# Optimization experiments

Measured on AMD Instinct MI355X. Metric: run time of the kernel, lower is better.

Reference implementation:

```python
import jax, jax.numpy as jnp
import numpy as np

B, S, D = 8, 1024, 512          # batch, seq_len, embed_dim
H = 8                            # num_heads
KD = D                           # key_dim = embed_dim (per source)
DM = H * KD                      # internal d_model = 4096
FF = 2048                        # dense_dim
EPS = 1e-3                       # keras LayerNormalization default epsilon


def glorot(key, shape):
    fan_in, fan_out = shape[0], shape[1]
    lim = np.sqrt(6.0 / (fan_in + fan_out)).astype(np.float32)
    return jax.random.uniform(key, shape, jnp.float32, -lim, lim)


def setup_inputs() -> dict:
    key = jax.random.key(0)
    ks = jax.random.split(key, 8)
    return {
        "inputs": jax.random.normal(ks[0], (B, S, D), jnp.float32),
        "w_q": glorot(ks[1], (D, DM)), "b_q": jnp.zeros((DM,), jnp.float32),
        "w_k": glorot(ks[2], (D, DM)), "b_k": jnp.zeros((DM,), jnp.float32),
        "w_v": glorot(ks[3], (D, DM)), "b_v": jnp.zeros((DM,), jnp.float32),
        "w_o": glorot(ks[4], (DM, D)), "b_o": jnp.zeros((D,), jnp.float32),
        "w1": glorot(ks[5], (D, FF)), "b1": jnp.zeros((FF,), jnp.float32),
        "w2": glorot(ks[6], (FF, D)), "b2": jnp.zeros((D,), jnp.float32),
        "g1": jnp.ones((D,), jnp.float32), "beta1": jnp.zeros((D,), jnp.float32),
        "g2": jnp.ones((D,), jnp.float32), "beta2": jnp.zeros((D,), jnp.float32),
    }


def _layernorm(x, gamma, beta):
    mu = jnp.mean(x, axis=-1, keepdims=True)
    var = jnp.mean(jnp.square(x - mu), axis=-1, keepdims=True)
    return (x - mu) * jax.lax.rsqrt(var + EPS) * gamma + beta


def reference(inputs, w_q, b_q, w_k, b_k, w_v, b_v, w_o, b_o,
              w1, b1, w2, b2, g1, beta1, g2, beta2):
    # --- custom multi-head self-attention ---
    q = (inputs @ w_q + b_q).reshape(B, S, H, KD)   # [B,S,H,KD]
    k = (inputs @ w_k + b_k).reshape(B, S, H, KD)
    v = (inputs @ w_v + b_v).reshape(B, S, H, KD)
    scale = jnp.sqrt(jnp.float32(KD))
    scores = jnp.einsum("bqhd,bkhd->bhqk", q, k) / scale   # [B,H,S,S]
    attn = jax.nn.softmax(scores, axis=-1)
    ctx = jnp.einsum("bhqk,bkhd->bqhd", attn, v).reshape(B, S, DM)
    attn_out = ctx @ w_o + b_o                               # [B,S,D]
    # --- residual + LN 1 ---
    proj_in = _layernorm(inputs + attn_out, g1, beta1)
    # --- FFN ---
    ffn = jax.nn.relu(proj_in @ w1 + b1) @ w2 + b2
    # --- residual + LN 2 ---
    return _layernorm(proj_in + ffn, g2, beta2)
```

## Files before the change

### kernel.cpp

```cpp
#include <hip/hip_runtime.h>
#include <stdint.h>

typedef __bf16 bf16_t;
typedef bf16_t bf16x8 __attribute__((ext_vector_type(8)));
typedef float floatx4 __attribute__((ext_vector_type(4)));

__device__ __forceinline__ unsigned short f2bf(float f) {
  union { float f; uint32_t u; } v; v.f = f;
  return (unsigned short)((v.u + 0x7fffu + ((v.u >> 16) & 1u)) >> 16);
}

#define GLD16(g, l)                                                            \
  __builtin_amdgcn_global_load_lds(                                            \
      (const __attribute__((address_space(1))) void*)(g),                      \
      (__attribute__((address_space(3))) void*)(l), 16, 0, 0)

__device__ __forceinline__ void xcd_swizzle(int& bx, int& by) {
  const int nx = gridDim.x;
  const int nwg = nx * gridDim.y;
  int id = blockIdx.y * nx + blockIdx.x;
  const int cpx = nwg >> 3;
  id = (id & 7) * cpx + (id >> 3);
  bx = id % nx;
  by = id / nx;
}

template <int BIAS_MODE, bool RELU, bool OUT_BF16>
__global__ __launch_bounds__(512, 2) void gemm256(
    const unsigned short* __restrict__ A, const unsigned short* __restrict__ Bt,
    void* __restrict__ C, const float* __restrict__ bias, int K, int lda,
    int ldb, int ldc, long sA, long sB, long sC) {
  __shared__ __align__(16) unsigned short As[2][256 * 64];
  __shared__ __align__(16) unsigned short Bs[2][256 * 64];
  int bx, by;
  xcd_swizzle(bx, by);
  const int tid = threadIdx.x;
  const int lane = tid & 63;
  const int wave = tid >> 6;
  const int quad = lane >> 4;
  const int l15 = lane & 15;
  const unsigned short* Ab = A + blockIdx.z * sA + (long)by * 256 * lda;
  const unsigned short* Bb = Bt + blockIdx.z * sB + (long)bx * 256 * ldb;
  const int wm = (wave & 1) << 7;
  const int wn = (wave >> 1) << 6;

  floatx4 acc[8][4] = {};

  const int sr = tid >> 3;
  const int sc = tid & 7;
  const int NT = K >> 6;

  auto stage = [&](int t, int buf) {
    const int kt = t << 6;
#pragma unroll
    for (int i = 0; i < 4; ++i) {
      int r = sr + i * 64;
      int gc = sc ^ (r & 7);
      GLD16(Ab + (long)r * lda + kt + gc * 8,
            &As[buf][(i * 64 + (wave << 3)) * 64]);
    }
#pragma unroll
    for (int i = 0; i < 4; ++i) {
      int r = sr + i * 64;
      int gc = sc ^ (r & 7);
      GLD16(Bb + (long)r * ldb + kt + gc * 8,
            &Bs[buf][(i * 64 + (wave << 3)) * 64]);
    }
  };

  stage(0, 0);
  stage(1, 1);
  asm volatile("s_waitcnt vmcnt(8)\n\ts_barrier" ::: "memory");

  int cur = 0;
  for (int t = 0; t < NT; ++t) {
    const unsigned short* Ap = As[cur];
    const unsigned short* Bp = Bs[cur];
    bf16x8 bF[2][2][2];
#pragma unroll
    for (int jh = 0; jh < 2; ++jh)
#pragma unroll
      for (int j2 = 0; j2 < 2; ++j2)
#pragma unroll
        for (int ks = 0; ks < 2; ++ks) {
          int row = wn + jh * 32 + j2 * 16 + l15;
          int sw = (ks * 4 + quad) ^ (row & 7);
          bF[jh][j2][ks] = *(const bf16x8*)(Bp + row * 64 + sw * 8);
        }
#pragma unroll
    for (int ih = 0; ih < 2; ++ih) {
      bf16x8 aF[4][2];
#pragma unroll
      for (int i4 = 0; i4 < 4; ++i4)
#pragma unroll
        for (int ks = 0; ks < 2; ++ks) {
          int row = wm + ih * 64 + i4 * 16 + l15;
          int sw = (ks * 4 + quad) ^ (row & 7);
          aF[i4][ks] = *(const bf16x8*)(Ap + row * 64 + sw * 8);
        }
#pragma unroll
      for (int jh = 0; jh < 2; ++jh) {
        __builtin_amdgcn_s_setprio(1);
#pragma unroll
        for (int j2 = 0; j2 < 2; ++j2)
#pragma unroll
          for (int i4 = 0; i4 < 4; ++i4)
#pragma unroll
            for (int ks = 0; ks < 2; ++ks)
              acc[ih * 4 + i4][jh * 2 + j2] =
                  __builtin_amdgcn_mfma_f32_16x16x32_bf16(
                      aF[i4][ks], bF[jh][j2][ks],
                      acc[ih * 4 + i4][jh * 2 + j2], 0, 0, 0);
        __builtin_amdgcn_s_setprio(0);
      }
    }
    if (t == NT - 1) break;
    asm volatile("s_waitcnt lgkmcnt(0)\n\ts_barrier" ::: "memory");
    if (t + 2 < NT) {
      stage(t + 2, cur);
      asm volatile("s_waitcnt vmcnt(8)\n\ts_barrier" ::: "memory");
    } else {
      asm volatile("s_waitcnt vmcnt(0)\n\ts_barrier" ::: "memory");
    }
    cur ^= 1;
  }

  const int rl = quad << 2;
  const int cl = l15;
#pragma unroll
  for (int i = 0; i < 8; ++i) {
#pragma unroll
    for (int j = 0; j < 4; ++j) {
#pragma unroll
      for (int rg = 0; rg < 4; ++rg) {
        int row = (by << 8) + wm + i * 16 + rl + rg;
        int col = (bx << 8) + wn + j * 16 + cl;
        float v = acc[i][j][rg];
        if (BIAS_MODE == 1) v += bias[col];
        if (BIAS_MODE == 2) v += bias[row];
        if (RELU) v = fmaxf(v, 0.0f);
        long idx = blockIdx.z * sC + (long)row * ldc + col;
        if (OUT_BF16)
          ((unsigned short*)C)[idx] = f2bf(v);
        else
          ((float*)C)[idx] = v;
      }
    }
  }
}

template <int BIAS_MODE, bool RELU, bool OUT_BF16>
__global__ __launch_bounds__(256, 2) void gemm128p(
    const unsigned short* __restrict__ A, const unsigned short* __restrict__ Bt,
    void* __restrict__ C, const float* __restrict__ bias, int K, int lda,
    int ldb, int ldc, long sA, long sB, long sC) {
  __shared__ __align__(16) unsigned short As[2][128 * 64];
  __shared__ __align__(16) unsigned short Bs[2][128 * 64];
  int bx, by;
  xcd_swizzle(bx, by);
  const int tid = threadIdx.x;
  const int lane = tid & 63;
  const int wave = tid >> 6;
  const int quad = lane >> 4;
  const int l15 = lane & 15;
  const unsigned short* Ab = A + blockIdx.z * sA + (long)by * 128 * lda;
  const unsigned short* Bb = Bt + blockIdx.z * sB + (long)bx * 128 * ldb;
  const int wm = (wave & 1) << 6;
  const int wn = (wave >> 1) << 6;

  floatx4 acc[4][4] = {};

  const int sr = tid >> 3;
  const int sc = tid & 7;
  const int NT = K >> 6;

  auto stage = [&](int t, int buf) {
    const int kt = t << 6;
#pragma unroll
    for (int i = 0; i < 4; ++i) {
      int r = sr + i * 32;
      int gc = sc ^ (r & 7);
      GLD16(Ab + (long)r * lda + kt + gc * 8,
            &As[buf][(i * 32 + (wave << 3)) * 64]);
    }
#pragma unroll
    for (int i = 0; i < 4; ++i) {
      int r = sr + i * 32;
      int gc = sc ^ (r & 7);
      GLD16(Bb + (long)r * ldb + kt + gc * 8,
            &Bs[buf][(i * 32 + (wave << 3)) * 64]);
    }
  };

  stage(0, 0);
  stage(1, 1);
  asm volatile("s_waitcnt vmcnt(8)\n\ts_barrier" ::: "memory");

  int cur = 0;
  for (int t = 0; t < NT; ++t) {
    const unsigned short* Ap = As[cur];
    const unsigned short* Bp = Bs[cur];
#pragma unroll
    for (int ks = 0; ks < 2; ++ks) {
      bf16x8 af[4], bfr[4];
#pragma unroll
      for (int i = 0; i < 4; ++i) {
        int row = wm + i * 16 + l15;
        int ch = (ks * 4 + quad) ^ (row & 7);
        af[i] = *(const bf16x8*)(Ap + row * 64 + ch * 8);
      }
#pragma unroll
      for (int j = 0; j < 4; ++j) {
        int row = wn + j * 16 + l15;
        int ch = (ks * 4 + quad) ^ (row & 7);
        bfr[j] = *(const bf16x8*)(Bp + row * 64 + ch * 8);
      }
      __builtin_amdgcn_s_setprio(1);
#pragma unroll
      for (int i = 0; i < 4; ++i)
#pragma unroll
        for (int j = 0; j < 4; ++j)
          acc[i][j] = __builtin_amdgcn_mfma_f32_16x16x32_bf16(af[i], bfr[j],
                                                              acc[i][j], 0, 0, 0);
      __builtin_amdgcn_s_setprio(0);
    }
    if (t == NT - 1) break;
    asm volatile("s_waitcnt lgkmcnt(0)\n\ts_barrier" ::: "memory");
    if (t + 2 < NT) {
      stage(t + 2, cur);
      asm volatile("s_waitcnt vmcnt(8)\n\ts_barrier" ::: "memory");
    } else {
      asm volatile("s_waitcnt vmcnt(0)\n\ts_barrier" ::: "memory");
    }
    cur ^= 1;
  }

  const int rl = quad << 2;
  const int cl = l15;
#pragma unroll
  for (int i = 0; i < 4; ++i) {
#pragma unroll
    for (int j = 0; j < 4; ++j) {
#pragma unroll
      for (int rg = 0; rg < 4; ++rg) {
        int row = (by << 7) + wm + i * 16 + rl + rg;
        int col = (bx << 7) + wn + j * 16 + cl;
        float v = acc[i][j][rg];
        if (BIAS_MODE == 1) v += bias[col];
        if (BIAS_MODE == 2) v += bias[row];
        if (RELU) v = fmaxf(v, 0.0f);
        long idx = blockIdx.z * sC + (long)row * ldc + col;
        if (OUT_BF16)
          ((unsigned short*)C)[idx] = f2bf(v);
        else
          ((float*)C)[idx] = v;
      }
    }
  }
}

__global__ __launch_bounds__(512, 2) void attn(
    const unsigned short* __restrict__ qk, const unsigned short* __restrict__ vt,
    unsigned short* __restrict__ ctx) {
  __shared__ unsigned short ldsK[2][32 * 512];
  __shared__ unsigned short ldsV[2][32 * 512];
  __shared__ unsigned short ldsP[128 * 40];
  __shared__ float ldsL[128];

  const int tid = threadIdx.x;
  const int lane = tid & 63;
  const int wave = tid >> 6;
  const int quad = lane >> 4;
  const int l15 = lane & 15;
  const int b = blockIdx.x >> 3;
  const int h = blockIdx.x & 7;
  const int qblk = blockIdx.y << 7;
  const float cs = 0.044194173824159216f * 1.4426950408889634f;

  bf16x8 qf[16];
  {
    const unsigned short* qp =
        qk + (long)(b * 1024 + qblk + wave * 16 + l15) * 8192 + h * 512 +
        (quad << 3);
#pragma unroll
    for (int ks = 0; ks < 16; ++ks) qf[ks] = *(const bf16x8*)(qp + ks * 32);
  }

  floatx4 o[32];
#pragma unroll
  for (int i = 0; i < 32; ++i) o[i] = floatx4{0.f, 0.f, 0.f, 0.f};
  floatx4 l_i = floatx4{0.f, 0.f, 0.f, 0.f};

  const int st_d = lane >> 2;
  const int st_kc = ((lane & 3) - (lane >> 3)) & 3;

  {
#pragma unroll
    for (int i = 0; i < 4; ++i) {
      int r = i * 8 + wave;
      int gc = (lane & ~7) | ((lane ^ r) & 7);
      GLD16(qk + (long)(b * 1024 + r) * 8192 + 4096 + h * 512 + gc * 8,
            ldsK[0] + r * 512);
    }
#pragma unroll
    for (int i = 0; i < 4; ++i) {
      int j = i * 8 + wave;
      GLD16(vt + (long)(b * 4096 + h * 512 + j * 16 + st_d) * 1024 + st_kc * 8,
            ldsV[0] + j * 512);
    }
  }
  __syncthreads();

  for (int kt = 0; kt < 32; ++kt) {
    const unsigned short* kb = ldsK[kt & 1];
    const unsigned short* vb = ldsV[kt & 1];
    if (kt + 1 < 32) {
#pragma unroll
      for (int i = 0; i < 4; ++i) {
        int r = i * 8 + wave;
        int gc = (lane & ~7) | ((lane ^ r) & 7);
        GLD16(qk + (long)(b * 1024 + (kt + 1) * 32 + r) * 8192 + 4096 +
                  h * 512 + gc * 8,
              ldsK[(kt + 1) & 1] + r * 512);
      }
#pragma unroll
      for (int i = 0; i < 4; ++i) {
        int j = i * 8 + wave;
        GLD16(vt + (long)(b * 4096 + h * 512 + j * 16 + st_d) * 1024 +
                  (kt + 1) * 32 + st_kc * 8,
              ldsV[(kt + 1) & 1] + j * 512);
      }
    }

    floatx4 s0 = floatx4{0.f, 0.f, 0.f, 0.f}, s1 = floatx4{0.f, 0.f, 0.f, 0.f};
#pragma unroll
    for (int ks = 0; ks < 16; ++ks) {
      int ch = ks * 4 + quad;
      int sw = (ch & ~7) | ((ch ^ l15) & 7);
      bf16x8 k0 = *(const bf16x8*)(kb + l15 * 512 + sw * 8);
      bf16x8 k1 = *(const bf16x8*)(kb + (16 + l15) * 512 + sw * 8);
      s0 = __builtin_amdgcn_mfma_f32_16x16x32_bf16(qf[ks], k0, s0, 0, 0, 0);
      s1 = __builtin_amdgcn_mfma_f32_16x16x32_bf16(qf[ks], k1, s1, 0, 0, 0);
    }

    {
      unsigned short* pw = ldsP + wave * 16 * 40;
      const int rb = quad << 2;
#pragma unroll
      for (int r = 0; r < 4; ++r) {
        float e0 = __builtin_amdgcn_exp2f(s0[r] * cs);
        float e1 = __builtin_amdgcn_exp2f(s1[r] * cs);
        l_i[r] += e0 + e1;
        pw[(rb + r) * 40 + l15] = f2bf(e0);
        pw[(rb + r) * 40 + 16 + l15] = f2bf(e1);
      }
    }
    asm volatile("s_waitcnt lgkmcnt(0)\n\ts_barrier" ::: "memory");

#pragma unroll
    for (int half = 0; half < 2; ++half) {
      bf16x8 pf[4];
#pragma unroll
      for (int q4 = 0; q4 < 4; ++q4)
        pf[q4] = *(const bf16x8*)(ldsP + ((half * 4 + q4) * 16 + l15) * 40 +
                                  (quad << 3));
#pragma unroll
      for (int db = 0; db < 4; ++db) {
        int n = wave * 4 + db;
        bf16x8 vf = *(const bf16x8*)(
            vb + n * 512 + (l15 * 4 + ((quad + (l15 >> 1)) & 3)) * 8);
#pragma unroll
        for (int q4 = 0; q4 < 4; ++q4)
          o[(half * 4 + q4) * 4 + db] = __builtin_amdgcn_mfma_f32_16x16x32_bf16(
              pf[q4], vf, o[(half * 4 + q4) * 4 + db], 0, 0, 0);
      }
    }
    __syncthreads();
  }

#pragma unroll
  for (int r = 0; r < 4; ++r) {
    float rs = l_i[r];
    rs += __shfl_xor(rs, 1);
    rs += __shfl_xor(rs, 2);
    rs += __shfl_xor(rs, 4);
    rs += __shfl_xor(rs, 8);
    if (l15 == 0) ldsL[wave * 16 + (quad << 2) + r] = rs;
  }
  __syncthreads();

#pragma unroll
  for (int qb = 0; qb < 8; ++qb) {
    floatx4 lv = *(const floatx4*)(ldsL + qb * 16 + (quad << 2));
    floatx4 inv;
#pragma unroll
    for (int r = 0; r < 4; ++r) inv[r] = 1.0f / lv[r];
#pragma unroll
    for (int db = 0; db < 4; ++db) {
#pragma unroll
      for (int r = 0; r < 4; ++r) {
        long row = (long)(b * 1024 + qblk + qb * 16 + (quad << 2) + r);
        ctx[row * 4096 + h * 512 + wave * 64 + db * 16 + l15] =
            f2bf(o[qb * 4 + db][r] * inv[r]);
      }
    }
  }
}

template <int NPART, bool WB>
__global__ __launch_bounds__(256) void ln_reduce(
    const float* __restrict__ p, long sP, const float* __restrict__ bias,
    const float* __restrict__ resid, const float* __restrict__ gamma,
    const float* __restrict__ beta, float* __restrict__ of,
    unsigned short* __restrict__ ob) {
  const long row = blockIdx.x;
  const int c = threadIdx.x * 2;
  const float2 rv = ((const float2*)(resid + row * 512))[threadIdx.x];
  float x0 = bias[c] + rv.x;
  float x1 = bias[c + 1] + rv.y;
#pragma unroll
  for (int k = 0; k < NPART; ++k) {
    const float2 a = ((const float2*)(p + k * sP + row * 512))[threadIdx.x];
    x0 += a.x;
    x1 += a.y;
  }
  float s = x0 + x1;
  float ss = x0 * x0 + x1 * x1;
#pragma unroll
  for (int d = 1; d < 64; d <<= 1) {
    s += __shfl_xor(s, d);
    ss += __shfl_xor(ss, d);
  }
  __shared__ float ps[4], pq[4];
  const int wave = threadIdx.x >> 6;
  if ((threadIdx.x & 63) == 0) {
    ps[wave] = s;
    pq[wave] = ss;
  }
  __syncthreads();
  s = ps[0] + ps[1] + ps[2] + ps[3];
  ss = pq[0] + pq[1] + pq[2] + pq[3];
  const float mu = s * (1.0f / 512.0f);
  const float rstd = rsqrtf(ss * (1.0f / 512.0f) - mu * mu + 1e-3f);
  const float y0 = (x0 - mu) * rstd * gamma[c] + beta[c];
  const float y1 = (x1 - mu) * rstd * gamma[c + 1] + beta[c + 1];
  ((float2*)(of + row * 512))[threadIdx.x] = make_float2(y0, y1);
  if (WB) {
    ushort2 o2;
    o2.x = f2bf(y0);
    o2.y = f2bf(y1);
    ((ushort2*)(ob + row * 512))[threadIdx.x] = o2;
  }
}

__global__ __launch_bounds__(256) void cast_bf16(const float* __restrict__ in,
                                                 unsigned short* __restrict__ out,
                                                 int n) {
  int i = (blockIdx.x * 256 + threadIdx.x) * 4;
  if (i < n) {
    float4 v = *(const float4*)(in + i);
    ushort4 o;
    o.x = f2bf(v.x);
    o.y = f2bf(v.y);
    o.z = f2bf(v.z);
    o.w = f2bf(v.w);
    *(ushort4*)(out + i) = o;
  }
}

__global__ __launch_bounds__(256) void transpose_cast(const float* __restrict__ in,
                                                      unsigned short* __restrict__ out,
                                                      int R, int C) {
  __shared__ float tile[32][33];
  const int tx = threadIdx.x & 31, ty = threadIdx.x >> 5;
  const int c0 = blockIdx.x * 32, r0 = blockIdx.y * 32;
#pragma unroll
  for (int i = 0; i < 4; ++i)
    tile[ty + i * 8][tx] = in[(long)(r0 + ty + i * 8) * C + c0 + tx];
  __syncthreads();
#pragma unroll
  for (int i = 0; i < 4; ++i)
    out[(long)(c0 + ty + i * 8) * R + r0 + tx] = f2bf(tile[tx][ty + i * 8]);
}

extern "C" void kernel_launch(void* const* d_in, const int* in_sizes, int n_in,
                              void* d_out, int out_size, void* d_ws,
                              size_t ws_size, hipStream_t stream) {
  const float* x = (const float*)d_in[0];
  const float* w_q = (const float*)d_in[1];
  const float* b_q = (const float*)d_in[2];
  const float* w_k = (const float*)d_in[3];
  const float* b_k = (const float*)d_in[4];
  const float* w_v = (const float*)d_in[5];
  const float* b_v = (const float*)d_in[6];
  const float* w_o = (const float*)d_in[7];
  const float* b_o = (const float*)d_in[8];
  const float* w1 = (const float*)d_in[9];
  const float* b1 = (const float*)d_in[10];
  const float* w2 = (const float*)d_in[11];
  const float* b2 = (const float*)d_in[12];
  const float* g1 = (const float*)d_in[13];
  const float* be1 = (const float*)d_in[14];
  const float* g2 = (const float*)d_in[15];
  const float* be2 = (const float*)d_in[16];
  float* out = (float*)d_out;

  char* ws = (char*)d_ws;
  size_t off = 0;
  auto alloc = [&](size_t n) {
    char* p = ws + off;
    off += (n + 255) & ~(size_t)255;
    return p;
  };
  unsigned short* xb = (unsigned short*)alloc(8192ll * 512 * 2);
  unsigned short* wqk_t = (unsigned short*)alloc(8192ll * 512 * 2);
  unsigned short* wv_t = (unsigned short*)alloc(4096ll * 512 * 2);
  unsigned short* wo_t = (unsigned short*)alloc(512ll * 4096 * 2);
  unsigned short* w1_t = (unsigned short*)alloc(2048ll * 512 * 2);
  unsigned short* w2_t = (unsigned short*)alloc(512ll * 2048 * 2);
  float* bqk = (float*)alloc(8192ll * 4);
  unsigned short* qkb = (unsigned short*)alloc(4096ll * 8192 * 2);
  unsigned short* vtb = (unsigned short*)alloc(4ll * 4096 * 1024 * 2);
  unsigned short* ctxf = (unsigned short*)alloc(8192ll * 4096 * 2);
  float* proj = (float*)alloc(8192ll * 512 * 4);
  unsigned short* projb = xb;
  unsigned short* h1 = qkb;
  float* pOP = (float*)qkb;
  float* pF2 = (float*)ctxf;

  hipMemcpyAsync(bqk, b_q, 4096 * 4, hipMemcpyDeviceToDevice, stream);
  hipMemcpyAsync(bqk + 4096, b_k, 4096 * 4, hipMemcpyDeviceToDevice, stream);

  cast_bf16<<<4096, 256, 0, stream>>>(x, xb, 8192 * 512);
  transpose_cast<<<dim3(128, 16), 256, 0, stream>>>(w_q, wqk_t, 512, 4096);
  transpose_cast<<<dim3(128, 16), 256, 0, stream>>>(w_k, wqk_t + 4096ll * 512, 512, 4096);
  transpose_cast<<<dim3(128, 16), 256, 0, stream>>>(w_v, wv_t, 512, 4096);
  transpose_cast<<<dim3(16, 128), 256, 0, stream>>>(w_o, wo_t, 4096, 512);
  transpose_cast<<<dim3(64, 16), 256, 0, stream>>>(w1, w1_t, 512, 2048);
  transpose_cast<<<dim3(16, 64), 256, 0, stream>>>(w2, w2_t, 2048, 512);

  for (int g = 0; g < 2; ++g) {
    const unsigned short* xg = xb + (long)g * 4096 * 512;
    gemm256<1, false, true><<<dim3(32, 16, 1), 512, 0, stream>>>(
        xg, wqk_t, qkb, bqk, 512, 512, 512, 8192, 0, 0, 0);
    gemm256<2, false, true><<<dim3(4, 16, 4), 512, 0, stream>>>(
        wv_t, xg, vtb, b_v, 512, 512, 512, 1024, 0, 1024ll * 512,
        4096ll * 1024);
    attn<<<dim3(32, 8), 512, 0, stream>>>(qkb, vtb, ctxf + (long)g * 4096 * 4096);
  }
  gemm128p<0, false, false><<<dim3(4, 64, 2), 256, 0, stream>>>(
      ctxf, wo_t, pOP, nullptr, 2048, 4096, 4096, 512, 2048, 2048,
      8192ll * 512);
  ln_reduce<2, true><<<8192, 256, 0, stream>>>(pOP, 8192ll * 512, b_o, x, g1,
                                               be1, proj, projb);
  gemm256<1, true, true><<<dim3(8, 32, 1), 512, 0, stream>>>(
      projb, w1_t, h1, b1, 512, 512, 512, 2048, 0, 0, 0);
  gemm128p<0, false, false><<<dim3(4, 64, 2), 256, 0, stream>>>(
      h1, w2_t, pF2, nullptr, 1024, 2048, 2048, 512, 1024, 1024,
      8192ll * 512);
  ln_reduce<2, false><<<8192, 256, 0, stream>>>(pF2, 8192ll * 512, b2, proj,
                                                g2, be2, out, nullptr);
}
```

Baseline: 479.1 us.

## Store split-K partials in bf16 and hoist V projection out of batch loop

The split-K partial outputs of the output-projection and second FFN GEMMs are now written as bf16 instead of fp32, and the LayerNorm reduce kernel reads and widens them. This halves partial-sum traffic. The V projection is now computed once for all 8 batches in a single larger launch before the loop, with the V buffer doubled in size, which cuts launches and raises the grid size. The cost is bf16 rounding of the partials before they are summed, which adds error ahead of the LayerNorm.

```diff
diff --git a/kernel.cpp b/kernel.cpp
--- a/kernel.cpp
+++ b/kernel.cpp
@@ -8,6 +8,12 @@
 __device__ __forceinline__ unsigned short f2bf(float f) {
   union { float f; uint32_t u; } v; v.f = f;
   return (unsigned short)((v.u + 0x7fffu + ((v.u >> 16) & 1u)) >> 16);
+}
+
+__device__ __forceinline__ float bf2f(unsigned short b) {
+  union { uint32_t u; float f; } v;
+  v.u = (uint32_t)b << 16;
+  return v.f;
 }
 
 #define GLD16(g, l)                                                            \
@@ -409,10 +415,10 @@
 
 template <int NPART, bool WB>
 __global__ __launch_bounds__(256) void ln_reduce(
-    const float* __restrict__ p, long sP, const float* __restrict__ bias,
-    const float* __restrict__ resid, const float* __restrict__ gamma,
-    const float* __restrict__ beta, float* __restrict__ of,
-    unsigned short* __restrict__ ob) {
+    const unsigned short* __restrict__ p, long sP,
+    const float* __restrict__ bias, const float* __restrict__ resid,
+    const float* __restrict__ gamma, const float* __restrict__ beta,
+    float* __restrict__ of, unsigned short* __restrict__ ob) {
   const long row = blockIdx.x;
   const int c = threadIdx.x * 2;
   const float2 rv = ((const float2*)(resid + row * 512))[threadIdx.x];
@@ -420,9 +426,9 @@
   float x1 = bias[c + 1] + rv.y;
 #pragma unroll
   for (int k = 0; k < NPART; ++k) {
-    const float2 a = ((const float2*)(p + k * sP + row * 512))[threadIdx.x];
-    x0 += a.x;
-    x1 += a.y;
+    const ushort2 a = ((const ushort2*)(p + k * sP + row * 512))[threadIdx.x];
+    x0 += bf2f(a.x);
+    x1 += bf2f(a.y);
   }
   float s = x0 + x1;
   float ss = x0 * x0 + x1 * x1;
@@ -520,13 +526,13 @@
   unsigned short* w2_t = (unsigned short*)alloc(512ll * 2048 * 2);
   float* bqk = (float*)alloc(8192ll * 4);
   unsigned short* qkb = (unsigned short*)alloc(4096ll * 8192 * 2);
-  unsigned short* vtb = (unsigned short*)alloc(4ll * 4096 * 1024 * 2);
+  unsigned short* vtb = (unsigned short*)alloc(8ll * 4096 * 1024 * 2);
   unsigned short* ctxf = (unsigned short*)alloc(8192ll * 4096 * 2);
   float* proj = (float*)alloc(8192ll * 512 * 4);
   unsigned short* projb = xb;
   unsigned short* h1 = qkb;
-  float* pOP = (float*)qkb;
-  float* pF2 = (float*)ctxf;
+  unsigned short* pOP = qkb;
+  unsigned short* pF2 = (unsigned short*)ctxf;
 
   hipMemcpyAsync(bqk, b_q, 4096 * 4, hipMemcpyDeviceToDevice, stream);
   hipMemcpyAsync(bqk + 4096, b_k, 4096 * 4, hipMemcpyDeviceToDevice, stream);
@@ -539,23 +545,25 @@
   transpose_cast<<<dim3(64, 16), 256, 0, stream>>>(w1, w1_t, 512, 2048);
   transpose_cast<<<dim3(16, 64), 256, 0, stream>>>(w2, w2_t, 2048, 512);
 
+  gemm256<2, false, true><<<dim3(4, 16, 8), 512, 0, stream>>>(
+      wv_t, xb, vtb, b_v, 512, 512, 512, 1024, 0, 1024ll * 512,
+      4096ll * 1024);
+
   for (int g = 0; g < 2; ++g) {
     const unsigned short* xg = xb + (long)g * 4096 * 512;
     gemm256<1, false, true><<<dim3(32, 16, 1), 512, 0, stream>>>(
         xg, wqk_t, qkb, bqk, 512, 512, 512, 8192, 0, 0, 0);
-    gemm256<2, false, true><<<dim3(4, 16, 4), 512, 0, stream>>>(
-        wv_t, xg, vtb, b_v, 512, 512, 512, 1024, 0, 1024ll * 512,
-        4096ll * 1024);
-    attn<<<dim3(32, 8), 512, 0, stream>>>(qkb, vtb, ctxf + (long)g * 4096 * 4096);
-  }
-  gemm128p<0, false, false><<<dim3(4, 64, 2), 256, 0, stream>>>(
+    attn<<<dim3(32, 8), 512, 0, stream>>>(
+        qkb, vtb + (long)g * 4 * 4096 * 1024, ctxf + (long)g * 4096 * 4096);
+  }
+  gemm128p<0, false, true><<<dim3(4, 64, 2), 256, 0, stream>>>(
       ctxf, wo_t, pOP, nullptr, 2048, 4096, 4096, 512, 2048, 2048,
       8192ll * 512);
   ln_reduce<2, true><<<8192, 256, 0, stream>>>(pOP, 8192ll * 512, b_o, x, g1,
                                                be1, proj, projb);
   gemm256<1, true, true><<<dim3(8, 32, 1), 512, 0, stream>>>(
       projb, w1_t, h1, b1, 512, 512, 512, 2048, 0, 0, 0);
-  gemm128p<0, false, false><<<dim3(4, 64, 2), 256, 0, stream>>>(
+  gemm128p<0, false, true><<<dim3(4, 64, 2), 256, 0, stream>>>(
       h1, w2_t, pF2, nullptr, 1024, 2048, 2048, 512, 1024, 1024,
       8192ll * 512);
   ln_reduce<2, false><<<8192, 256, 0, stream>>>(pF2, 8192ll * 512, b2, proj,
```

After: 473.2 us. Within noise of the previous version (-1.2%).
